# Optimization experiments

Hardware: AMD Instinct MI355X
Metric: run time of the kernel (lower is better)

Reference implementation:

```python
import jax, jax.numpy as jnp
import numpy as np

N = 50000      # num nodes
E = 1_600_000  # num edges (avg degree 32)
L = 200_000    # num label edges to decode
D_IN, H1, H2 = 256, 128, 64


def setup_inputs() -> dict:
    key = jax.random.key(0)
    ks = jax.random.split(key, 20)

    def w(k, fan_in, fan_out):
        return jax.random.normal(k, (fan_in, fan_out), jnp.float32) * (1.0 / np.sqrt(fan_in))

    return {
        'x': jax.random.normal(ks[0], (N, D_IN), jnp.float32),
        'prev0': jax.random.normal(ks[1], (N, H1), jnp.float32),
        'prev1': jax.random.normal(ks[2], (N, H2), jnp.float32),
        'Wpre1': w(ks[3], D_IN, 256), 'bpre1': jnp.zeros((256,), jnp.float32),
        'Wpre2': w(ks[4], 256, 128),  'bpre2': jnp.zeros((128,), jnp.float32),
        'Wc1': w(ks[5], 128, H1),     'bc1': jnp.zeros((H1,), jnp.float32),
        'Wc2': w(ks[6], H1, H2),      'bc2': jnp.zeros((H2,), jnp.float32),
        'Wm1': w(ks[7], 2 * H1, H1),  'bm1': jnp.zeros((H1,), jnp.float32),
        'Wm2': w(ks[8], 2 * H2, H2),  'bm2': jnp.zeros((H2,), jnp.float32),
        'Wpost': w(ks[9], H2, 2),     'bpost': jnp.zeros((2,), jnp.float32),
        'edge_index': jax.random.randint(ks[10], (2, E), 0, N, jnp.int32),
        'edge_label_index': jax.random.randint(ks[11], (2, L), 0, N, jnp.int32),
    }


def _gcn_conv(h, W, b, src, dst, n):
    """PyG GCNConv: add self-loops, sym-normalize D^-1/2 (A+I) D^-1/2 (X W) + b."""
    hw = h @ W                                   # [N, out]
    deg = jax.ops.segment_sum(jnp.ones_like(src, jnp.float32), dst, num_segments=n) + 1.0
    dinv = jax.lax.rsqrt(deg)                    # [N]
    norm = dinv[src] * dinv[dst]                 # [E]
    agg = jax.ops.segment_sum(hw[src] * norm[:, None], dst, num_segments=n)
    agg = agg + hw * (dinv * dinv)[:, None]      # self-loop term
    return agg + b


def reference(x, prev0, prev1, Wpre1, bpre1, Wpre2, bpre2, Wc1, bc1, Wc2, bc2,
              Wm1, bm1, Wm2, bm2, Wpost, bpost, edge_index, edge_label_index):
    # isnap > 0 with update='mlp'; dropout p=0.0 -> identity
    src, dst = edge_index[0], edge_index[1]
    n = x.shape[0]

    h = jax.nn.relu(x @ Wpre1 + bpre1)
    h = jax.nn.relu(h @ Wpre2 + bpre2)

    h = jax.nn.relu(_gcn_conv(h, Wc1, bc1, src, dst, n))
    h = jnp.concatenate([h, prev0], axis=1) @ Wm1 + bm1   # temporal MLP update 1
    emb0 = h

    h = jax.nn.relu(_gcn_conv(h, Wc2, bc2, src, dst, n))
    h = jnp.concatenate([h, prev1], axis=1) @ Wm2 + bm2   # temporal MLP update 2
    emb1 = h

    # hadamard edge decode
    h_had = emb1[edge_label_index[0]] * emb1[edge_label_index[1]]  # [L, H2]
    pred = jnp.sum(h_had @ Wpost + bpost, axis=-1)                 # [L]
    return pred, emb0, emb1
```

## Files before the change

kernel.cpp:

```cpp
#include <hip/hip_runtime.h>
#include <hip/hip_bf16.h>


typedef unsigned short ushort_t;
typedef __attribute__((ext_vector_type(8))) short s8v;
typedef __attribute__((ext_vector_type(4))) float f4;

#define BSHIFT 8

__device__ __forceinline__ ushort_t f2bf(float v) {
    unsigned u = __float_as_uint(v);
    return (ushort_t)((u + 0x7FFFu + ((u >> 16) & 1u)) >> 16);
}

__device__ __forceinline__ s8v cvt8(f4 v0, f4 v1) {
    ushort_t hb[8];
    hb[0] = f2bf(v0.x); hb[1] = f2bf(v0.y); hb[2] = f2bf(v0.z); hb[3] = f2bf(v0.w);
    hb[4] = f2bf(v1.x); hb[5] = f2bf(v1.y); hb[6] = f2bf(v1.z); hb[7] = f2bf(v1.w);
    return *(s8v*)hb;
}

__device__ __forceinline__ size_t swzidx(int row, int k, int Wd) {
    int p = (((k & 63) >> 3) ^ (row & 7));
    return (size_t)row * Wd + (k & ~63) + p * 8 + (k & 7);
}

__device__ __forceinline__ void dma16(const ushort_t* g, ushort_t* l) {
    __builtin_amdgcn_global_load_lds(
        (const __attribute__((address_space(1))) unsigned int*)g,
        (__attribute__((address_space(3))) unsigned int*)l, 16, 0, 0);
}

__device__ __forceinline__ void add8(float* acc, uint4 u, float m) {
    acc[0] = fmaf(__uint_as_float(u.x << 16), m, acc[0]);
    acc[1] = fmaf(__uint_as_float(u.x & 0xFFFF0000u), m, acc[1]);
    acc[2] = fmaf(__uint_as_float(u.y << 16), m, acc[2]);
    acc[3] = fmaf(__uint_as_float(u.y & 0xFFFF0000u), m, acc[3]);
    acc[4] = fmaf(__uint_as_float(u.z << 16), m, acc[4]);
    acc[5] = fmaf(__uint_as_float(u.z & 0xFFFF0000u), m, acc[5]);
    acc[6] = fmaf(__uint_as_float(u.w << 16), m, acc[6]);
    acc[7] = fmaf(__uint_as_float(u.w & 0xFFFF0000u), m, acc[7]);
}

template <int W>
__global__ __launch_bounds__(256) void f2bswz_kernel(const float* __restrict__ in,
                                                     ushort_t* __restrict__ out, size_t n) {
    size_t i = ((size_t)blockIdx.x * 256 + threadIdx.x) * 8;
    if (i + 8 > n) return;
    f4 v0 = *(const f4*)&in[i];
    f4 v1 = *(const f4*)&in[i + 4];
    int row = (int)(i / W), k = (int)(i % W);
    *(s8v*)&out[swzidx(row, k, W)] = cvt8(v0, v1);
}

template <int BN, int KW, int K1, bool A1F32, bool RELU, bool SCALE, bool DUAL,
          int OUTMODE, bool SWZO>
__global__ __launch_bounds__(256, 2) void gemm_lds(
    const float* __restrict__ A1f, const ushort_t* __restrict__ A1h,
    const ushort_t* __restrict__ A2h,
    const ushort_t* __restrict__ Wt,
    const float* __restrict__ bias, const float* __restrict__ rowscale,
    float* __restrict__ Cf, ushort_t* __restrict__ Ch,
    int M, int Nout)
{
    constexpr int NT = BN / 32;
    constexpr int K2 = KW - K1;
    __shared__ ushort_t Abuf[64 * 64];
    __shared__ ushort_t Bbuf[BN * 64];

    const int tid  = threadIdx.x;
    const int lane = tid & 63;
    const int w    = tid >> 6;
    const int wr   = w >> 1, wc = w & 1;
    const int rbase = blockIdx.y * 64;
    const int bn    = blockIdx.x * BN;

    f4 acc[2][NT];
    const f4 zero = {0.f, 0.f, 0.f, 0.f};
#pragma unroll
    for (int mi = 0; mi < 2; ++mi)
#pragma unroll
        for (int ni = 0; ni < NT; ++ni) acc[mi][ni] = zero;

    for (int kt = 0; kt < KW; kt += 64) {
        if constexpr (A1F32) {
#pragma unroll
            for (int j = 0; j < 2; ++j) {
                const int c2 = tid + j * 256;
                const int row = c2 >> 3, c = c2 & 7;
                const int gr = min(rbase + row, M - 1);
                const float* p = &A1f[(size_t)gr * K1 + kt + c * 8];
                const int pc = c ^ (row & 7);
                *(s8v*)&Abuf[row * 64 + pc * 8] = cvt8(*(const f4*)p, *(const f4*)(p + 4));
            }
        } else {
#pragma unroll
            for (int i = 0; i < 2; ++i) {
                const int s = w * 2 + i;
                const int row = s * 8 + (lane >> 3);
                const int c = lane & 7;
                const int gr = min(rbase + row, M - 1);
                const ushort_t* g;
                if (DUAL && kt >= K1) g = &A2h[(size_t)gr * K2 + (kt - K1) + c * 8];
                else                  g = &A1h[(size_t)gr * K1 + kt + c * 8];
                dma16(g, &Abuf[s * 512]);
            }
        }
#pragma unroll
        for (int i = 0; i < NT; ++i) {
            const int s = w * NT + i;
            const int colr = s * 8 + (lane >> 3);
            const int c = lane & 7;
            dma16(&Wt[(size_t)(bn + colr) * KW + kt + c * 8], &Bbuf[s * 512]);
        }
        __syncthreads();
#pragma unroll
        for (int ks = 0; ks < 2; ++ks) {
            const int c = ks * 4 + (lane >> 4);
            s8v bfrag[NT];
#pragma unroll
            for (int ni = 0; ni < NT; ++ni) {
                const int colr = wc * (NT * 16) + ni * 16 + (lane & 15);
                bfrag[ni] = *(const s8v*)&Bbuf[colr * 64 + (c ^ (colr & 7)) * 8];
            }
#pragma unroll
            for (int mi = 0; mi < 2; ++mi) {
                const int row = wr * 32 + mi * 16 + (lane & 15);
                const s8v af = *(const s8v*)&Abuf[row * 64 + (c ^ (row & 7)) * 8];
#pragma unroll
                for (int ni = 0; ni < NT; ++ni)
                    acc[mi][ni] = __builtin_amdgcn_mfma_f32_16x16x32_bf16(af, bfrag[ni], acc[mi][ni], 0, 0, 0);
            }
        }
        __syncthreads();
    }

#pragma unroll
    for (int mi = 0; mi < 2; ++mi) {
#pragma unroll
        for (int reg = 0; reg < 4; ++reg) {
            const int row = rbase + wr * 32 + mi * 16 + (lane >> 4) * 4 + reg;
            if (row >= M) continue;
            const float rs = SCALE ? rowscale[row] : 1.f;
#pragma unroll
            for (int ni = 0; ni < NT; ++ni) {
                const int col = bn + wc * (NT * 16) + ni * 16 + (lane & 15);
                float v = acc[mi][ni][reg];
                if (SCALE) v *= rs;
                if (bias) v += bias[col];
                if (RELU) v = fmaxf(v, 0.f);
                const size_t oidx = SWZO ? swzidx(row, col, Nout) : ((size_t)row * Nout + col);
                if constexpr (OUTMODE == 2) {
                    Ch[oidx] = f2bf(v);
                } else if constexpr (OUTMODE == 3) {
                    Cf[(size_t)row * Nout + col] = v;
                    Ch[oidx] = f2bf(v);
                } else {
                    Cf[(size_t)row * Nout + col] = v;
                }
            }
        }
    }
}

struct WDesc { const float* W; ushort_t* h; int K; int No; };
struct WAll { WDesc d[6]; };

__global__ void wtcvt_kernel(WAll wa) {
    WDesc d = wa.d[blockIdx.y];
    int e = blockIdx.x * blockDim.x + threadIdx.x;
    if (e >= d.K * d.No) return;
    int k = e / d.No, n = e - k * d.No;
    d.h[swzidx(n, k, d.K)] = f2bf(d.W[e]);
}

__global__ __launch_bounds__(256) void bcount_kernel(const int* __restrict__ dst,
                                                     int* __restrict__ bcount, int E, int NB) {
    __shared__ int cnt[256];
    const int t = threadIdx.x;
    if (t < NB) cnt[t] = 0;
    __syncthreads();
    for (int e = blockIdx.x * 256 + t; e < E; e += gridDim.x * 256)
        atomicAdd(&cnt[dst[e] >> BSHIFT], 1);
    __syncthreads();
    if (t < NB && cnt[t]) atomicAdd(&bcount[t], cnt[t]);
}

__global__ __launch_bounds__(256) void bscan_kernel(const int* __restrict__ bcount,
                                                    int* __restrict__ bbase,
                                                    int* __restrict__ bcursor, int NB, int E) {
    __shared__ int s[256];
    const int t = threadIdx.x;
    s[t] = (t < NB) ? bcount[t] : 0;
    __syncthreads();
    for (int off = 1; off < 256; off <<= 1) {
        int v = (t >= off) ? s[t - off] : 0;
        __syncthreads();
        s[t] += v;
        __syncthreads();
    }
    int excl = t ? s[t - 1] : 0;
    if (t < NB) { bbase[t] = excl; bcursor[t] = excl; }
    if (t == 0) bbase[NB] = E;
}

__global__ __launch_bounds__(256) void bpart_kernel(const int* __restrict__ src,
                                                    const int* __restrict__ dst,
                                                    int* __restrict__ bcursor,
                                                    unsigned* __restrict__ packed, int E, int NB) {
    __shared__ int cnt[256];
    __shared__ int cur[256];
    const int t = threadIdx.x;
    const int beg = blockIdx.x * 8192;
    const int end = min(beg + 8192, E);
    if (t < NB) cnt[t] = 0;
    __syncthreads();
    for (int e = beg + t; e < end; e += 256) atomicAdd(&cnt[dst[e] >> BSHIFT], 1);
    __syncthreads();
    if (t < NB && cnt[t]) cur[t] = atomicAdd(&bcursor[t], cnt[t]);
    __syncthreads();
    for (int e = beg + t; e < end; e += 256) {
        int d = dst[e];
        int b = d >> BSHIFT;
        int pos = atomicAdd(&cur[b], 1);
        packed[pos] = (unsigned)src[e] | ((unsigned)(d & ((1 << BSHIFT) - 1)) << 16);
    }
}

__global__ __launch_bounds__(256) void bbuild_kernel(const int* __restrict__ bbase,
                                                     const unsigned* __restrict__ packed,
                                                     int* __restrict__ col,
                                                     int* __restrict__ rowstart,
                                                     float* __restrict__ dinv, int N, int E) {
    __shared__ int ncnt[256];
    __shared__ int s[256];
    __shared__ int ncur[256];
    const int b = blockIdx.x;
    const int t = threadIdx.x;
    const int beg = bbase[b], end = bbase[b + 1];
    const int node0 = b << BSHIFT;
    const int nInB = min(256, N - node0);
    ncnt[t] = 0;
    __syncthreads();
    for (int e = beg + t; e < end; e += 256) atomicAdd(&ncnt[packed[e] >> 16], 1);
    __syncthreads();
    s[t] = ncnt[t];
    __syncthreads();
    for (int off = 1; off < 256; off <<= 1) {
        int v = (t >= off) ? s[t - off] : 0;
        __syncthreads();
        s[t] += v;
        __syncthreads();
    }
    int excl = t ? s[t - 1] : 0;
    if (t < nInB) {
        rowstart[node0 + t] = beg + excl;
        dinv[node0 + t] = rsqrtf((float)ncnt[t] + 1.0f);
    }
    ncur[t] = beg + excl;
    __syncthreads();
    for (int e = beg + t; e < end; e += 256) {
        unsigned p = packed[e];
        int pos = atomicAdd(&ncur[p >> 16], 1);
        col[pos] = (int)(p & 0xFFFFu);
    }
    if (b == 0 && t == 0) rowstart[N] = E;
}

template <int F>
__global__ __launch_bounds__(256) void gather4_kernel(const int* __restrict__ rowstart,
                                                      const int* __restrict__ col,
                                                      const float* __restrict__ dinv,
                                                      const ushort_t* __restrict__ hws,
                                                      const float* __restrict__ bias,
                                                      ushort_t* __restrict__ aggb, int N) {
    const int wave = threadIdx.x >> 6;
    const int lane = threadIdx.x & 63;
    const int d = blockIdx.x * 4 + wave;
    if (d >= N) return;
    const int beg = rowstart[d], end = rowstart[d + 1];
    const float dd = dinv[d];
    const uint4* rowp = (const uint4*)hws;

    if (F == 128) {
        const int q = lane >> 4;
        const int c = lane & 15;
        float acc[8] = {};
        uint4 sv = rowp[(size_t)d * 16 + c];
        if (q == 0) add8(acc, sv, 1.f);
        for (int e0 = beg; e0 < end; e0 += 64) {
            int nid = (e0 + lane < end) ? col[e0 + lane] : 0;
            int cnt = min(64, end - e0);
            for (int jj = 0; jj < cnt; jj += 4) {
                int s = __shfl(nid, jj + q);
                float m = (jj + q < cnt) ? 1.f : 0.f;
                uint4 u = rowp[(size_t)s * 16 + c];
                add8(acc, u, m);
            }
        }
#pragma unroll
        for (int i = 0; i < 8; ++i) {
            acc[i] += __shfl_down(acc[i], 32);
            acc[i] += __shfl_down(acc[i], 16);
        }
        if (q == 0) {
            f4 b0 = *(const f4*)&bias[c * 8];
            f4 b1 = *(const f4*)&bias[c * 8 + 4];
            float r[8];
            r[0] = fmaxf(acc[0] * dd + b0.x, 0.f); r[1] = fmaxf(acc[1] * dd + b0.y, 0.f);
            r[2] = fmaxf(acc[2] * dd + b0.z, 0.f); r[3] = fmaxf(acc[3] * dd + b0.w, 0.f);
            r[4] = fmaxf(acc[4] * dd + b1.x, 0.f); r[5] = fmaxf(acc[5] * dd + b1.y, 0.f);
            r[6] = fmaxf(acc[6] * dd + b1.z, 0.f); r[7] = fmaxf(acc[7] * dd + b1.w, 0.f);
            uint4 o;
            o.x = (unsigned)f2bf(r[0]) | ((unsigned)f2bf(r[1]) << 16);
            o.y = (unsigned)f2bf(r[2]) | ((unsigned)f2bf(r[3]) << 16);
            o.z = (unsigned)f2bf(r[4]) | ((unsigned)f2bf(r[5]) << 16);
            o.w = (unsigned)f2bf(r[6]) | ((unsigned)f2bf(r[7]) << 16);
            const int g = c >> 3;
            const int ch = (c & 7) ^ (d & 7);
            ((uint4*)aggb)[(size_t)d * 16 + g * 8 + ch] = o;
        }
    } else {
        const int q = lane >> 3;
        const int c = lane & 7;
        float acc[8] = {};
        uint4 sv = rowp[(size_t)d * 8 + c];
        if (q == 0) add8(acc, sv, 1.f);
        for (int e0 = beg; e0 < end; e0 += 64) {
            int nid = (e0 + lane < end) ? col[e0 + lane] : 0;
            int cnt = min(64, end - e0);
            for (int jj = 0; jj < cnt; jj += 8) {
                int s = __shfl(nid, jj + q);
                float m = (jj + q < cnt) ? 1.f : 0.f;
                uint4 u = rowp[(size_t)s * 8 + c];
                add8(acc, u, m);
            }
        }
#pragma unroll
        for (int i = 0; i < 8; ++i) {
            acc[i] += __shfl_down(acc[i], 32);
            acc[i] += __shfl_down(acc[i], 16);
            acc[i] += __shfl_down(acc[i], 8);
        }
        if (q == 0) {
            f4 b0 = *(const f4*)&bias[c * 8];
            f4 b1 = *(const f4*)&bias[c * 8 + 4];
            float r[8];
            r[0] = fmaxf(acc[0] * dd + b0.x, 0.f); r[1] = fmaxf(acc[1] * dd + b0.y, 0.f);
            r[2] = fmaxf(acc[2] * dd + b0.z, 0.f); r[3] = fmaxf(acc[3] * dd + b0.w, 0.f);
            r[4] = fmaxf(acc[4] * dd + b1.x, 0.f); r[5] = fmaxf(acc[5] * dd + b1.y, 0.f);
            r[6] = fmaxf(acc[6] * dd + b1.z, 0.f); r[7] = fmaxf(acc[7] * dd + b1.w, 0.f);
            uint4 o;
            o.x = (unsigned)f2bf(r[0]) | ((unsigned)f2bf(r[1]) << 16);
            o.y = (unsigned)f2bf(r[2]) | ((unsigned)f2bf(r[3]) << 16);
            o.z = (unsigned)f2bf(r[4]) | ((unsigned)f2bf(r[5]) << 16);
            o.w = (unsigned)f2bf(r[6]) | ((unsigned)f2bf(r[7]) << 16);
            const int ch = c ^ (d & 7);
            ((uint4*)aggb)[(size_t)d * 8 + ch] = o;
        }
    }
}

__global__ __launch_bounds__(256) void decode8_kernel(const ushort_t* __restrict__ emb1b,
                                                      const int* __restrict__ eli,
                                                      const float* __restrict__ Wpost,
                                                      const float* __restrict__ bpost,
                                                      float* __restrict__ pred, int L) {
    const int wave = threadIdx.x >> 6;
    const int lane = threadIdx.x & 63;
    const int l8 = (blockIdx.x * 4 + wave) * 8;
    if (l8 >= L) return;
    const int q = lane >> 3;
    const int c = lane & 7;
    const int l = min(l8 + q, L - 1);
    const int s = eli[l];
    const int d = eli[L + l];
    const uint4* rowp = (const uint4*)emb1b;
    uint4 ua = rowp[(size_t)s * 8 + c];
    uint4 ub = rowp[(size_t)d * 8 + c];
    f4 w0 = *(const f4*)&Wpost[c * 16];
    f4 w1 = *(const f4*)&Wpost[c * 16 + 4];
    f4 w2 = *(const f4*)&Wpost[c * 16 + 8];
    f4 w3 = *(const f4*)&Wpost[c * 16 + 12];
    float p = 0.f;
    p += __uint_as_float(ua.x << 16) * __uint_as_float(ub.x << 16) * (w0.x + w0.y);
    p += __uint_as_float(ua.x & 0xFFFF0000u) * __uint_as_float(ub.x & 0xFFFF0000u) * (w0.z + w0.w);
    p += __uint_as_float(ua.y << 16) * __uint_as_float(ub.y << 16) * (w1.x + w1.y);
    p += __uint_as_float(ua.y & 0xFFFF0000u) * __uint_as_float(ub.y & 0xFFFF0000u) * (w1.z + w1.w);
    p += __uint_as_float(ua.z << 16) * __uint_as_float(ub.z << 16) * (w2.x + w2.y);
    p += __uint_as_float(ua.z & 0xFFFF0000u) * __uint_as_float(ub.z & 0xFFFF0000u) * (w2.z + w2.w);
    p += __uint_as_float(ua.w << 16) * __uint_as_float(ub.w << 16) * (w3.x + w3.y);
    p += __uint_as_float(ua.w & 0xFFFF0000u) * __uint_as_float(ub.w & 0xFFFF0000u) * (w3.z + w3.w);
    p += __shfl_down(p, 4);
    p += __shfl_down(p, 2);
    p += __shfl_down(p, 1);
    if (c == 0 && l8 + q < L) pred[l8 + q] = p + bpost[0] + bpost[1];
}

extern "C" void kernel_launch(void* const* d_in, const int* in_sizes, int n_in,
                              void* d_out, int out_size, void* d_ws, size_t ws_size,
                              hipStream_t stream) {
    const float* x     = (const float*)d_in[0];
    const float* prev0 = (const float*)d_in[1];
    const float* prev1 = (const float*)d_in[2];
    const float* Wpre1 = (const float*)d_in[3];
    const float* bpre1 = (const float*)d_in[4];
    const float* Wpre2 = (const float*)d_in[5];
    const float* bpre2 = (const float*)d_in[6];
    const float* Wc1   = (const float*)d_in[7];
    const float* bc1   = (const float*)d_in[8];
    const float* Wc2   = (const float*)d_in[9];
    const float* bc2   = (const float*)d_in[10];
    const float* Wm1   = (const float*)d_in[11];
    const float* bm1   = (const float*)d_in[12];
    const float* Wm2   = (const float*)d_in[13];
    const float* bm2   = (const float*)d_in[14];
    const float* Wpost = (const float*)d_in[15];
    const float* bpost = (const float*)d_in[16];
    const int* edge_index = (const int*)d_in[17];
    const int* eli        = (const int*)d_in[18];

    const int N = in_sizes[0] / 256;
    const int E = in_sizes[17] / 2;
    const int L = in_sizes[18] / 2;
    const int NB = (N + 255) >> BSHIFT;

    const int* src = edge_index;
    const int* dst = edge_index + E;

    float* out  = (float*)d_out;
    float* pred = out;
    float* emb0 = out + L;
    float* emb1 = out + L + (size_t)N * 128;

    float* ws = (float*)d_ws;
    unsigned* packed = (unsigned*)ws;
    ushort_t* h1h   = (ushort_t*)ws;
    ushort_t* hws1b = (ushort_t*)ws;
    ushort_t* emb0b = (ushort_t*)ws;
    ushort_t* emb1b = (ushort_t*)ws;
    ushort_t* agg1b = (ushort_t*)(ws + (size_t)64 * N);
    ushort_t* hws2b = (ushort_t*)(ws + (size_t)64 * N);
    ushort_t* agg2b = (ushort_t*)(ws + (size_t)96 * N);
    ushort_t* h2b   = (ushort_t*)(ws + (size_t)128 * N);
    ushort_t* p0b   = (ushort_t*)(ws + (size_t)192 * N);
    ushort_t* p1b   = (ushort_t*)(ws + (size_t)256 * N);
    int*      col   = (int*)(ws + (size_t)288 * N);

    size_t o = (size_t)320 * N;
    int* rowstart = (int*)(ws + o);         o += ((size_t)N + 4) & ~(size_t)3;
    float* dinv = ws + o;                   o += ((size_t)N + 3) & ~(size_t)3;
    int* bbase = (int*)(ws + o);            o += 260;
    int* bcursor = (int*)(ws + o);          o += 260;
    int* bcount = (int*)(ws + o);           o += 260;
    ushort_t* wb = (ushort_t*)(ws + o);

    ushort_t* wpre1t = wb + 0;
    ushort_t* wpre2t = wb + 65536;
    ushort_t* wc1t   = wb + 98304;
    ushort_t* wm1t   = wb + 114688;
    ushort_t* wc2t   = wb + 147456;
    ushort_t* wm2t   = wb + 155648;

    {
        size_t n0 = (size_t)N * 128, n1 = (size_t)N * 64;
        f2bswz_kernel<128><<<(int)((n0 / 8 + 255) / 256), 256, 0, stream>>>(prev0, p0b, n0);
        f2bswz_kernel<64><<<(int)((n1 / 8 + 255) / 256), 256, 0, stream>>>(prev1, p1b, n1);
    }

    hipMemsetAsync(bcount, 0, (size_t)NB * sizeof(int), stream);
    bcount_kernel<<<1024, 256, 0, stream>>>(dst, bcount, E, NB);
    bscan_kernel<<<1, 256, 0, stream>>>(bcount, bbase, bcursor, NB, E);
    bpart_kernel<<<(E + 8191) / 8192, 256, 0, stream>>>(src, dst, bcursor, packed, E, NB);
    bbuild_kernel<<<NB, 256, 0, stream>>>(bbase, packed, col, rowstart, dinv, N, E);

    WAll wa;
    wa.d[0] = {Wpre1, wpre1t, 256, 256};
    wa.d[1] = {Wpre2, wpre2t, 256, 128};
    wa.d[2] = {Wc1,   wc1t,   128, 128};
    wa.d[3] = {Wm1,   wm1t,   256, 128};
    wa.d[4] = {Wc2,   wc2t,   128, 64};
    wa.d[5] = {Wm2,   wm2t,   128, 64};
    wtcvt_kernel<<<dim3(256, 6), 256, 0, stream>>>(wa);

    const int gy = (N + 63) / 64;

    gemm_lds<128, 256, 256, true, true, false, false, 2, true><<<dim3(2, gy), 256, 0, stream>>>(
        x, nullptr, nullptr, wpre1t, bpre1, nullptr, nullptr, h1h, N, 256);
    gemm_lds<128, 256, 256, false, true, false, false, 2, true><<<dim3(1, gy), 256, 0, stream>>>(
        nullptr, h1h, nullptr, wpre2t, bpre2, nullptr, nullptr, h2b, N, 128);
    gemm_lds<128, 128, 128, false, false, true, false, 2, false><<<dim3(1, gy), 256, 0, stream>>>(
        nullptr, h2b, nullptr, wc1t, nullptr, dinv, nullptr, hws1b, N, 128);
    gather4_kernel<128><<<(N + 3) / 4, 256, 0, stream>>>(rowstart, col, dinv, hws1b, bc1, agg1b, N);
    gemm_lds<128, 256, 128, false, false, false, true, 3, true><<<dim3(1, gy), 256, 0, stream>>>(
        nullptr, agg1b, p0b, wm1t, bm1, nullptr, emb0, emb0b, N, 128);
    gemm_lds<64, 128, 128, false, false, true, false, 2, false><<<dim3(1, gy), 256, 0, stream>>>(
        nullptr, emb0b, nullptr, wc2t, nullptr, dinv, nullptr, hws2b, N, 64);
    gather4_kernel<64><<<(N + 3) / 4, 256, 0, stream>>>(rowstart, col, dinv, hws2b, bc2, agg2b, N);
    gemm_lds<64, 128, 64, false, false, false, true, 3, false><<<dim3(1, gy), 256, 0, stream>>>(
        nullptr, agg2b, p1b, wm2t, bm2, nullptr, emb1, emb1b, N, 64);
    decode8_kernel<<<(L + 31) / 32, 256, 0, stream>>>(emb1b, eli, Wpost, bpost, pred, L);
}
```

Baseline: 288.4 us.

## Pipeline neighbor-row gathers through LDS with multi-slot async DMA prefetch

Rewrites the sparse aggregation kernel so that each wave streams neighbor rows into a 5-slot LDS ring buffer using direct global-to-LDS loads. Four groups stay in flight while one is consumed, and a vmcnt wait enforces the ordering. Column indices are fetched 256 at a time instead of 64. The aim is to hide gather latency with more memory-level parallelism, at the cost of 20KB of LDS per block, which may cut occupancy, and of dummy self-row loads that pad out the pipeline.

```diff
diff --git a/kernel.cpp b/kernel.cpp
--- a/kernel.cpp
+++ b/kernel.cpp
@@ -268,12 +268,15 @@
 }
 
 template <int F>
-__global__ __launch_bounds__(256) void gather4_kernel(const int* __restrict__ rowstart,
+__global__ __launch_bounds__(256) void gatherp_kernel(const int* __restrict__ rowstart,
                                                       const int* __restrict__ col,
                                                       const float* __restrict__ dinv,
                                                       const ushort_t* __restrict__ hws,
                                                       const float* __restrict__ bias,
                                                       ushort_t* __restrict__ aggb, int N) {
+    constexpr int RPG = (F == 128) ? 4 : 8;
+    constexpr int RW  = F / 8;
+    __shared__ ushort_t lbuf[4][5][512];
     const int wave = threadIdx.x >> 6;
     const int lane = threadIdx.x & 63;
     const int d = blockIdx.x * 4 + wave;
@@ -281,23 +284,55 @@
     const int beg = rowstart[d], end = rowstart[d + 1];
     const float dd = dinv[d];
     const uint4* rowp = (const uint4*)hws;
+    const int q = (F == 128) ? (lane >> 4) : (lane >> 3);
+    const int c = (F == 128) ? (lane & 15) : (lane & 7);
+    ushort_t* myb = &lbuf[wave][0][0];
+
+    float acc[8] = {};
+    {
+        uint4 sv = rowp[(size_t)d * RW + c];
+        if (q == 0) add8(acc, sv, 1.f);
+    }
+
+    for (int e0 = beg; e0 < end; e0 += 256) {
+        const int scdeg = min(256, end - e0);
+        const int G = (scdeg + RPG - 1) / RPG;
+        int nid0, nid1, nid2, nid3;
+        {
+            int e = e0 + lane;           nid0 = (e < end) ? col[e] : 0;
+            e = e0 + 64 + lane;          nid1 = (e < end) ? col[e] : 0;
+            e = e0 + 128 + lane;         nid2 = (e < end) ? col[e] : 0;
+            e = e0 + 192 + lane;         nid3 = (e < end) ? col[e] : 0;
+        }
+        auto issue = [&](int g, int slot) {
+            const int jj = g * RPG;
+            const int ch = jj >> 6, off = jj & 63;
+            int nn = (ch == 0) ? nid0 : (ch == 1) ? nid1 : (ch == 2) ? nid2 : nid3;
+            int s = __shfl(nn, off + q);
+            int sv = (jj + q < scdeg) ? s : d;
+            dma16((const ushort_t*)&rowp[(size_t)sv * RW + c], myb + slot * 512);
+        };
+#pragma unroll
+        for (int p = 0; p < 4; ++p) {
+            if (p < G) issue(p, p);
+            else       dma16((const ushort_t*)&rowp[(size_t)d * RW + c], myb + p * 512);
+        }
+        int wslot = 4, rslot = 0;
+        for (int g = 0; g < G; ++g) {
+            if (g + 4 < G) issue(g + 4, wslot);
+            else           dma16((const ushort_t*)&rowp[(size_t)d * RW + c], myb + wslot * 512);
+            asm volatile("s_waitcnt vmcnt(4)" ::: "memory");
+            __builtin_amdgcn_sched_barrier(0);
+            uint4 u = *(const uint4*)(myb + rslot * 512 + lane * 8);
+            float m = (g * RPG + q < scdeg) ? 1.f : 0.f;
+            add8(acc, u, m);
+            if (++wslot == 5) wslot = 0;
+            if (++rslot == 5) rslot = 0;
+        }
+        asm volatile("s_waitcnt vmcnt(0)" ::: "memory");
+    }
 
     if (F == 128) {
-        const int q = lane >> 4;
-        const int c = lane & 15;
-        float acc[8] = {};
-        uint4 sv = rowp[(size_t)d * 16 + c];
-        if (q == 0) add8(acc, sv, 1.f);
-        for (int e0 = beg; e0 < end; e0 += 64) {
-            int nid = (e0 + lane < end) ? col[e0 + lane] : 0;
-            int cnt = min(64, end - e0);
-            for (int jj = 0; jj < cnt; jj += 4) {
-                int s = __shfl(nid, jj + q);
-                float m = (jj + q < cnt) ? 1.f : 0.f;
-                uint4 u = rowp[(size_t)s * 16 + c];
-                add8(acc, u, m);
-            }
-        }
 #pragma unroll
         for (int i = 0; i < 8; ++i) {
             acc[i] += __shfl_down(acc[i], 32);
@@ -316,26 +351,11 @@
             o.y = (unsigned)f2bf(r[2]) | ((unsigned)f2bf(r[3]) << 16);
             o.z = (unsigned)f2bf(r[4]) | ((unsigned)f2bf(r[5]) << 16);
             o.w = (unsigned)f2bf(r[6]) | ((unsigned)f2bf(r[7]) << 16);
-            const int g = c >> 3;
+            const int g2 = c >> 3;
             const int ch = (c & 7) ^ (d & 7);
-            ((uint4*)aggb)[(size_t)d * 16 + g * 8 + ch] = o;
+            ((uint4*)aggb)[(size_t)d * 16 + g2 * 8 + ch] = o;
         }
     } else {
-        const int q = lane >> 3;
-        const int c = lane & 7;
-        float acc[8] = {};
-        uint4 sv = rowp[(size_t)d * 8 + c];
-        if (q == 0) add8(acc, sv, 1.f);
-        for (int e0 = beg; e0 < end; e0 += 64) {
-            int nid = (e0 + lane < end) ? col[e0 + lane] : 0;
-            int cnt = min(64, end - e0);
-            for (int jj = 0; jj < cnt; jj += 8) {
-                int s = __shfl(nid, jj + q);
-                float m = (jj + q < cnt) ? 1.f : 0.f;
-                uint4 u = rowp[(size_t)s * 8 + c];
-                add8(acc, u, m);
-            }
-        }
 #pragma unroll
         for (int i = 0; i < 8; ++i) {
             acc[i] += __shfl_down(acc[i], 32);
@@ -491,12 +511,12 @@
         nullptr, h1h, nullptr, wpre2t, bpre2, nullptr, nullptr, h2b, N, 128);
     gemm_lds<128, 128, 128, false, false, true, false, 2, false><<<dim3(1, gy), 256, 0, stream>>>(
         nullptr, h2b, nullptr, wc1t, nullptr, dinv, nullptr, hws1b, N, 128);
-    gather4_kernel<128><<<(N + 3) / 4, 256, 0, stream>>>(rowstart, col, dinv, hws1b, bc1, agg1b, N);
+    gatherp_kernel<128><<<(N + 3) / 4, 256, 0, stream>>>(rowstart, col, dinv, hws1b, bc1, agg1b, N);
     gemm_lds<128, 256, 128, false, false, false, true, 3, true><<<dim3(1, gy), 256, 0, stream>>>(
         nullptr, agg1b, p0b, wm1t, bm1, nullptr, emb0, emb0b, N, 128);
     gemm_lds<64, 128, 128, false, false, true, false, 2, false><<<dim3(1, gy), 256, 0, stream>>>(
         nullptr, emb0b, nullptr, wc2t, nullptr, dinv, nullptr, hws2b, N, 64);
-    gather4_kernel<64><<<(N + 3) / 4, 256, 0, stream>>>(rowstart, col, dinv, hws2b, bc2, agg2b, N);
+    gatherp_kernel<64><<<(N + 3) / 4, 256, 0, stream>>>(rowstart, col, dinv, hws2b, bc2, agg2b, N);
     gemm_lds<64, 128, 64, false, false, false, true, 3, false><<<dim3(1, gy), 256, 0, stream>>>(
         nullptr, agg2b, p1b, wm2t, bm2, nullptr, emb1, emb1b, N, 64);
     decode8_kernel<<<(L + 31) / 32, 256, 0, stream>>>(emb1b, eli, Wpost, bpost, pred, L);
```

After: 311.7 us. 1.08x slower.
